# Kernel optimization log

Hardware: AMD Instinct MI355X
Metric: run time of the kernel (lower is better)

The kernel has to match this reference:

```python
import jax, jax.numpy as jnp
import numpy as np
from jax import lax

DIM = 128
TOPW = 4
SCALE = DIM ** (-0.5)


def setup_inputs() -> dict:
    key = jax.random.key(0)
    kq, ki = jax.random.split(key)
    query = jax.random.normal(kq, (4, 4096, DIM), dtype=jnp.float32)
    image = jax.random.normal(ki, (4, 8192, DIM), dtype=jnp.float32)
    return {"query": query, "image": image}


def reference(query, image):
    # diff_routing=False: inputs are detached in torch; no effect on fwd values.
    # attn: (b, Nq, mn) = scaled QK^T
    attn = jnp.einsum('bqc,bmc->bqm', query, image) * SCALE
    _, topw_index = lax.top_k(attn, TOPW)  # (b, Nq, topw)
    return topw_index
```

## Files before the change

kernel.cpp:

```cpp
#include <hip/hip_runtime.h>
#include <float.h>
#include <stdint.h>


#define NBATCH 4
#define NQ 4096
#define NM 8192
#define KD 128

typedef unsigned short ushort_t;
typedef __attribute__((ext_vector_type(8))) short bf16x8;
typedef __attribute__((ext_vector_type(4))) float f32x4;

#define BETTER64(v, i, w, j) (((v) > (w)) || ((v) == (w) && (i) < (j)))

__device__ inline float fmed3(float a, float b, float c) {
#if __has_builtin(__builtin_amdgcn_fmed3f)
  return __builtin_amdgcn_fmed3f(a, b, c);
#else
  return fmaxf(fminf(a, b), fminf(fmaxf(a, b), c));
#endif
}

__device__ inline ushort_t f2bf(float f) {
  unsigned u = __float_as_uint(f);
  u += 0x7fffu + ((u >> 16) & 1u);
  return (ushort_t)(u >> 16);
}

__device__ inline unsigned pk2(float a, float b) {
  return (unsigned)f2bf(a) | ((unsigned)f2bf(b) << 16);
}

__global__ __launch_bounds__(256) void wr_cvt(const float* __restrict__ qry,
                                              const float* __restrict__ img,
                                              ushort_t* __restrict__ qb,
                                              int4* __restrict__ ib) {
  const int t = (int)blockIdx.x * 256 + (int)threadIdx.x;
  if (t < 524288) {
    const int b = t >> 17;
    const int tt = t & 131071;
    const int tile = tt >> 9;
    const int n = tt & 511;
    const int l = n & 63;
    const int m = tile * 32 + (n >> 8) * 16 + (l & 15);
    const int k0 = ((n >> 6) & 3) * 32 + ((l >> 4) & 3) * 8;
    const float* src = img + ((size_t)(b * NM + m)) * KD + k0;
    const float4 v0 = *(const float4*)(src);
    const float4 v1 = *(const float4*)(src + 4);
    int4 o;
    o.x = (int)pk2(v0.x, v0.y);
    o.y = (int)pk2(v0.z, v0.w);
    o.z = (int)pk2(v1.x, v1.y);
    o.w = (int)pk2(v1.z, v1.w);
    ib[t] = o;
  } else {
    const int u = t - 524288;
    const float4 v0 = ((const float4*)qry)[2 * u];
    const float4 v1 = ((const float4*)qry)[2 * u + 1];
    int4 o;
    o.x = (int)pk2(v0.x, v0.y);
    o.y = (int)pk2(v0.z, v0.w);
    o.z = (int)pk2(v1.x, v1.y);
    o.w = (int)pk2(v1.z, v1.w);
    ((int4*)qb)[u] = o;
  }
}

__global__ __launch_bounds__(512, 1) void wr_mfma(const float* __restrict__ qry,
                                                  const float* __restrict__ img,
                                                  const ushort_t* __restrict__ qb,
                                                  const int4* __restrict__ ib,
                                                  int* __restrict__ out) {
  const int bid = (int)blockIdx.x;
  const int b = (bid & 7) >> 1;
  const int qt = ((bid >> 3) << 1) | (bid & 1);
  const int qbase = qt * 64;

  const int tid = (int)threadIdx.x;
  const int lane = tid & 63;
  const int w = tid >> 6;
  const int q15 = lane & 15;
  const int quad = lane >> 4;

  const ushort_t* Qb = qb + ((size_t)b * NQ + qbase) * KD;
  const int4* ibc = ib + (size_t)b * 131072;

  bf16x8 bfrag[4][4];
#pragma unroll
  for (int s = 0; s < 4; ++s)
#pragma unroll
    for (int ks = 0; ks < 4; ++ks)
      bfrag[s][ks] =
          *(const bf16x8*)(Qb + (size_t)(s * 16 + q15) * KD + ks * 32 + quad * 8);

  float tch[4][4];
#pragma unroll
  for (int s = 0; s < 4; ++s)
#pragma unroll
    for (int e = 0; e < 4; ++e) tch[s][e] = -FLT_MAX;

  bf16x8 B0[4], B1[4], B2[4];

  auto loadH = [&](bf16x8* R, int h) {
    const int4* p = ibc + (((w * 64 + h) << 8) + lane);
#pragma unroll
    for (int ks = 0; ks < 4; ++ks) R[ks] = *(const bf16x8*)(p + ks * 64);
  };

  int hl = 3;
  int vb = 2047 - 4 * quad;

  auto step = [&](bf16x8* R) {
    f32x4 a[4];
#pragma unroll
    for (int s = 0; s < 4; ++s) a[s] = {0.f, 0.f, 0.f, 0.f};
#pragma unroll
    for (int ks = 0; ks < 4; ++ks)
#pragma unroll
      for (int s = 0; s < 4; ++s)
        a[s] = __builtin_amdgcn_mfma_f32_16x16x32_bf16(R[ks], bfrag[s][ks], a[s],
                                                       0, 0, 0);
    if (hl < 64) loadH(R, hl);
    ++hl;
#pragma unroll
    for (int s = 0; s < 4; ++s) {
#pragma unroll
      for (int r = 0; r < 4; ++r) {
        const unsigned kr = (unsigned)(vb - r);
        const float k =
            __uint_as_float((__float_as_uint(a[s][r]) & 0xFFFFF800u) | kr);
        tch[s][3] = fmed3(k, tch[s][2], tch[s][3]);
        tch[s][2] = fmed3(k, tch[s][1], tch[s][2]);
        tch[s][1] = fmed3(k, tch[s][0], tch[s][1]);
        tch[s][0] = fmaxf(tch[s][0], k);
      }
    }
    vb -= 16;
  };

  loadH(B0, 0);
  loadH(B1, 1);
  loadH(B2, 2);
  for (int g = 0; g < 21; ++g) { step(B0); step(B1); step(B2); }
  step(B0);

#pragma unroll
  for (int s = 0; s < 4; ++s) {
    float k4[4];
#pragma unroll
    for (int e = 0; e < 4; ++e) k4[e] = __shfl_down(tch[s][e], 32, 64);
#pragma unroll
    for (int e = 0; e < 4; ++e) {
      const float k = k4[e];
      tch[s][3] = fmed3(k, tch[s][2], tch[s][3]);
      tch[s][2] = fmed3(k, tch[s][1], tch[s][2]);
      tch[s][1] = fmed3(k, tch[s][0], tch[s][1]);
      tch[s][0] = fmaxf(tch[s][0], k);
    }
#pragma unroll
    for (int e = 0; e < 4; ++e) k4[e] = __shfl_down(tch[s][e], 16, 64);
#pragma unroll
    for (int e = 0; e < 4; ++e) {
      const float k = k4[e];
      tch[s][3] = fmed3(k, tch[s][2], tch[s][3]);
      tch[s][2] = fmed3(k, tch[s][1], tch[s][2]);
      tch[s][1] = fmed3(k, tch[s][0], tch[s][1]);
      tch[s][0] = fmaxf(tch[s][0], k);
    }
  }

  __shared__ float ck[64][33];
  __shared__ int top8[64][8];
  __shared__ double pd[64][8];
  __shared__ int pi[64][8];

  if (lane < 16) {
#pragma unroll
    for (int s = 0; s < 4; ++s)
#pragma unroll
      for (int e = 0; e < 4; ++e) ck[s * 16 + q15][w * 4 + e] = tch[s][e];
  }
  __syncthreads();

  for (int p = tid; p < 2048; p += 512) {
    const int q = p >> 5;
    const int j = p & 31;
    const float k = ck[q][j];
    int rank = 0;
#pragma unroll 8
    for (int i = 0; i < 32; ++i) {
      const float o = ck[q][i];
      rank += (o > k) || (o == k && i < j);
    }
    if (rank < 8) {
      const unsigned bits = __float_as_uint(k);
      top8[q][rank] = (j >> 2) * 1024 + 2047 - (int)(bits & 0x7FFu);
    }
  }
  __syncthreads();

  {
    const int q = tid >> 3;
    const int slot = tid & 7;
    const int m = top8[q][slot];
    const float* qrow = qry + ((size_t)b * NQ + qbase + q) * KD;
    const float* irow = img + ((size_t)b * NM + m) * KD;
    double s0 = 0.0, s1 = 0.0, s2 = 0.0, s3 = 0.0;
#pragma unroll
    for (int k = 0; k < KD; k += 4) {
      const float4 xv = *(const float4*)(qrow + k);
      const float4 yv = *(const float4*)(irow + k);
      s0 = fma((double)xv.x, (double)yv.x, s0);
      s1 = fma((double)xv.y, (double)yv.y, s1);
      s2 = fma((double)xv.z, (double)yv.z, s2);
      s3 = fma((double)xv.w, (double)yv.w, s3);
    }
    pd[q][slot] = (s0 + s1) + (s2 + s3);
    pi[q][slot] = m;
  }
  __syncthreads();

  if (tid < 64) {
    const int q = tid;
    double fv[4];
    int fi[4];
#pragma unroll
    for (int e = 0; e < 4; ++e) { fv[e] = -DBL_MAX; fi[e] = 0x7fffffff; }
    for (int sl = 0; sl < 8; ++sl) {
      const double v = pd[q][sl];
      const int m = pi[q][sl];
      const bool b0 = BETTER64(v, m, fv[0], fi[0]);
      const bool b1 = BETTER64(v, m, fv[1], fi[1]);
      const bool b2 = BETTER64(v, m, fv[2], fi[2]);
      const bool b3 = BETTER64(v, m, fv[3], fi[3]);
      fv[3] = b2 ? fv[2] : (b3 ? v : fv[3]);
      fi[3] = b2 ? fi[2] : (b3 ? m : fi[3]);
      fv[2] = b1 ? fv[1] : (b2 ? v : fv[2]);
      fi[2] = b1 ? fi[1] : (b2 ? m : fi[2]);
      fv[1] = b0 ? fv[0] : (b1 ? v : fv[1]);
      fi[1] = b0 ? fi[0] : (b1 ? m : fi[1]);
      fv[0] = b0 ? v : fv[0];
      fi[0] = b0 ? m : fi[0];
    }
    int4 o;
    o.x = fi[0]; o.y = fi[1]; o.z = fi[2]; o.w = fi[3];
    *(int4*)(out + ((size_t)b * NQ + qbase + q) * 4) = o;
  }
}

#define QT 64
#define MT 128
#define KC 64
#define NTHREADS 512

__global__ __launch_bounds__(NTHREADS) void wr_main(const float* __restrict__ qry,
                                                    const float* __restrict__ img,
                                                    int* __restrict__ out) {
  __shared__ __align__(16) float A_lds[KD * QT];
  __shared__ __align__(16) float B_lds[KC * MT];

  const int t = (int)threadIdx.x;
  const int b = (int)blockIdx.x >> 6;
  const int qbase = ((int)blockIdx.x & 63) * QT;

  const float* qp = qry + ((size_t)b * NQ + qbase) * KD;
  const float* ip = img + (size_t)b * NM * KD;

  {
    const int r = t >> 3;
    const int kc = t & 7;
    const float* src = qp + (size_t)r * KD;
#pragma unroll
    for (int i = 0; i < 4; ++i) {
      const int k0 = kc * 4 + i * 32;
      const float4 v = *(const float4*)(src + k0);
      A_lds[(k0 + 0) * QT + r] = v.x;
      A_lds[(k0 + 1) * QT + r] = v.y;
      A_lds[(k0 + 2) * QT + r] = v.z;
      A_lds[(k0 + 3) * QT + r] = v.w;
    }
  }

  const int qi = t >> 5;
  const int mi = t & 31;

  float tv[4][4];
  int ti[4][4];
#pragma unroll
  for (int j = 0; j < 4; ++j)
#pragma unroll
    for (int s = 0; s < 4; ++s) { tv[j][s] = -FLT_MAX; ti[j][s] = 0x7fffffff; }

  for (int tile = 0; tile < NM / MT; ++tile) {
    const int mbase = tile * MT;
    float acc[4][4];
#pragma unroll
    for (int j = 0; j < 4; ++j)
#pragma unroll
      for (int s = 0; s < 4; ++s) acc[j][s] = 0.0f;

    for (int kb = 0; kb < KD; kb += KC) {
      __syncthreads();
      {
        const int r = t >> 2;
        const int kc = t & 3;
        const float* src = ip + (size_t)(mbase + r) * KD + kb;
#pragma unroll
        for (int i = 0; i < 4; ++i) {
          const int k0 = kc * 4 + i * 16;
          const float4 v = *(const float4*)(src + k0);
          B_lds[(k0 + 0) * MT + r] = v.x;
          B_lds[(k0 + 1) * MT + r] = v.y;
          B_lds[(k0 + 2) * MT + r] = v.z;
          B_lds[(k0 + 3) * MT + r] = v.w;
        }
      }
      __syncthreads();

#pragma unroll 8
      for (int k = 0; k < KC; ++k) {
        const float4 av = *(const float4*)&A_lds[(kb + k) * QT + qi * 4];
        const float4 bv = *(const float4*)&B_lds[k * MT + mi * 4];
        acc[0][0] = fmaf(av.x, bv.x, acc[0][0]);
        acc[0][1] = fmaf(av.x, bv.y, acc[0][1]);
        acc[0][2] = fmaf(av.x, bv.z, acc[0][2]);
        acc[0][3] = fmaf(av.x, bv.w, acc[0][3]);
        acc[1][0] = fmaf(av.y, bv.x, acc[1][0]);
        acc[1][1] = fmaf(av.y, bv.y, acc[1][1]);
        acc[1][2] = fmaf(av.y, bv.z, acc[1][2]);
        acc[1][3] = fmaf(av.y, bv.w, acc[1][3]);
        acc[2][0] = fmaf(av.z, bv.x, acc[2][0]);
        acc[2][1] = fmaf(av.z, bv.y, acc[2][1]);
        acc[2][2] = fmaf(av.z, bv.z, acc[2][2]);
        acc[2][3] = fmaf(av.z, bv.w, acc[2][3]);
        acc[3][0] = fmaf(av.w, bv.x, acc[3][0]);
        acc[3][1] = fmaf(av.w, bv.y, acc[3][1]);
        acc[3][2] = fmaf(av.w, bv.z, acc[3][2]);
        acc[3][3] = fmaf(av.w, bv.w, acc[3][3]);
      }
    }

#pragma unroll
    for (int j = 0; j < 4; ++j) {
#pragma unroll
      for (int s = 0; s < 4; ++s) {
        const float v = acc[j][s];
        const int m = mbase + mi * 4 + s;
        const bool b0 = v > tv[j][0];
        const bool b1 = v > tv[j][1];
        const bool b2 = v > tv[j][2];
        const bool b3 = v > tv[j][3];
        tv[j][3] = b2 ? tv[j][2] : (b3 ? v : tv[j][3]);
        ti[j][3] = b2 ? ti[j][2] : (b3 ? m : ti[j][3]);
        tv[j][2] = b1 ? tv[j][1] : (b2 ? v : tv[j][2]);
        ti[j][2] = b1 ? ti[j][1] : (b2 ? m : ti[j][2]);
        tv[j][1] = b0 ? tv[j][0] : (b1 ? v : tv[j][1]);
        ti[j][1] = b0 ? ti[j][0] : (b1 ? m : ti[j][1]);
        tv[j][0] = b0 ? v : tv[j][0];
        ti[j][0] = b0 ? m : ti[j][0];
      }
    }
  }

  __syncthreads();
  int* idx_lds = (int*)B_lds;
#pragma unroll
  for (int j = 0; j < 4; ++j)
#pragma unroll
    for (int s = 0; s < 4; ++s)
      idx_lds[(qi * 4 + j) * 128 + mi * 4 + s] = ti[j][s];
  __syncthreads();

  double* pv = (double*)A_lds;
  int* piL = (int*)(A_lds + 4096);
  {
    const int r = t >> 3;
    const int slot = t & 7;
    const float* qrow = qp + (size_t)r * KD;
    double bv[4];
    int bi[4];
#pragma unroll
    for (int e = 0; e < 4; ++e) { bv[e] = -DBL_MAX; bi[e] = 0x7fffffff; }

    for (int c = 0; c < 16; ++c) {
      const int m = idx_lds[r * 128 + slot * 16 + c];
      const float* irow = ip + (size_t)m * KD;
      double s0 = 0.0, s1 = 0.0, s2 = 0.0, s3 = 0.0;
#pragma unroll
      for (int k = 0; k < KD; k += 4) {
        const float4 xv = *(const float4*)(qrow + k);
        const float4 yv = *(const float4*)(irow + k);
        s0 = fma((double)xv.x, (double)yv.x, s0);
        s1 = fma((double)xv.y, (double)yv.y, s1);
        s2 = fma((double)xv.z, (double)yv.z, s2);
        s3 = fma((double)xv.w, (double)yv.w, s3);
      }
      const double v = (s0 + s1) + (s2 + s3);
      const bool b0 = BETTER64(v, m, bv[0], bi[0]);
      const bool b1 = BETTER64(v, m, bv[1], bi[1]);
      const bool b2 = BETTER64(v, m, bv[2], bi[2]);
      const bool b3 = BETTER64(v, m, bv[3], bi[3]);
      bv[3] = b2 ? bv[2] : (b3 ? v : bv[3]);
      bi[3] = b2 ? bi[2] : (b3 ? m : bi[3]);
      bv[2] = b1 ? bv[1] : (b2 ? v : bv[2]);
      bi[2] = b1 ? bi[1] : (b2 ? m : bi[2]);
      bv[1] = b0 ? bv[0] : (b1 ? v : bv[1]);
      bi[1] = b0 ? bi[0] : (b1 ? m : bi[1]);
      bv[0] = b0 ? v : bv[0];
      bi[0] = b0 ? m : bi[0];
    }
#pragma unroll
    for (int e = 0; e < 4; ++e) {
      pv[t * 4 + e] = bv[e];
      piL[t * 4 + e] = bi[e];
    }
  }
  __syncthreads();

  if (t < QT) {
    double fv[4];
    int fi[4];
#pragma unroll
    for (int e = 0; e < 4; ++e) { fv[e] = -DBL_MAX; fi[e] = 0x7fffffff; }
    for (int sl = 0; sl < 8; ++sl) {
#pragma unroll
      for (int e = 0; e < 4; ++e) {
        const double v = pv[(t * 8 + sl) * 4 + e];
        const int m = piL[(t * 8 + sl) * 4 + e];
        const bool b0 = BETTER64(v, m, fv[0], fi[0]);
        const bool b1 = BETTER64(v, m, fv[1], fi[1]);
        const bool b2 = BETTER64(v, m, fv[2], fi[2]);
        const bool b3 = BETTER64(v, m, fv[3], fi[3]);
        fv[3] = b2 ? fv[2] : (b3 ? v : fv[3]);
        fi[3] = b2 ? fi[2] : (b3 ? m : fi[3]);
        fv[2] = b1 ? fv[1] : (b2 ? v : fv[2]);
        fi[2] = b1 ? fi[1] : (b2 ? m : fi[2]);
        fv[1] = b0 ? fv[0] : (b1 ? v : fv[1]);
        fi[1] = b0 ? fi[0] : (b1 ? m : fi[1]);
        fv[0] = b0 ? v : fv[0];
        fi[0] = b0 ? m : fi[0];
      }
    }
    int4 o;
    o.x = fi[0]; o.y = fi[1]; o.z = fi[2]; o.w = fi[3];
    *(int4*)(out + ((size_t)b * NQ + qbase + t) * 4) = o;
  }
}

extern "C" void kernel_launch(void* const* d_in, const int* in_sizes, int n_in,
                              void* d_out, int out_size, void* d_ws, size_t ws_size,
                              hipStream_t stream) {
  const float* qry = (const float*)d_in[0];
  const float* img = (const float*)d_in[1];
  int* out = (int*)d_out;

  const size_t qbBytes = (size_t)NBATCH * NQ * KD * sizeof(ushort_t);
  const size_t ibBytes = (size_t)NBATCH * NM * KD * sizeof(ushort_t);

  if (ws_size >= qbBytes + ibBytes) {
    ushort_t* qb = (ushort_t*)d_ws;
    int4* ib = (int4*)((char*)d_ws + qbBytes);
    wr_cvt<<<3072, 256, 0, stream>>>(qry, img, qb, ib);
    wr_mfma<<<256, 512, 0, stream>>>(qry, img, qb, ib, out);
  } else {
    wr_main<<<NBATCH * (NQ / QT), NTHREADS, 0, stream>>>(qry, img, out);
  }
}
```

Baseline: 133.6 us.

## Fuse bf16 conversion and MFMA top-k kernels with a grid-wide barrier

Merges the separate fp32-to-bf16 conversion kernel into the MFMA top-k kernel. All 256 blocks first convert a slice of the query and image data, then meet at a software grid barrier built from atomics in workspace memory before starting the matmul phase. This removes one kernel launch and the gap between launches. In exchange it adds a hipMemsetAsync per call and relies on all 256 blocks being resident at the same time, otherwise the barrier would deadlock.

Result: slower. 241.4 us (+80.7%).

```diff
diff --git a/kernel.cpp b/kernel.cpp
--- a/kernel.cpp
+++ b/kernel.cpp
@@ -32,12 +32,17 @@
   return (unsigned)f2bf(a) | ((unsigned)f2bf(b) << 16);
 }
 
-__global__ __launch_bounds__(256) void wr_cvt(const float* __restrict__ qry,
-                                              const float* __restrict__ img,
-                                              ushort_t* __restrict__ qb,
-                                              int4* __restrict__ ib) {
-  const int t = (int)blockIdx.x * 256 + (int)threadIdx.x;
-  if (t < 524288) {
+__global__ __launch_bounds__(512, 1) void wr_fused(
+    const float* __restrict__ qry, const float* __restrict__ img,
+    ushort_t* __restrict__ qb, int4* __restrict__ ib,
+    int* __restrict__ bar,
+    int* __restrict__ out) {
+  const int bid = (int)blockIdx.x;
+  const int tid = (int)threadIdx.x;
+
+#pragma unroll
+  for (int i = 0; i < 4; ++i) {
+    const int t = i * 131072 + bid * 512 + tid;
     const int b = t >> 17;
     const int tt = t & 131071;
     const int tile = tt >> 9;
@@ -54,8 +59,10 @@
     o.z = (int)pk2(v1.x, v1.y);
     o.w = (int)pk2(v1.z, v1.w);
     ib[t] = o;
-  } else {
-    const int u = t - 524288;
+  }
+#pragma unroll
+  for (int i = 0; i < 2; ++i) {
+    const int u = i * 131072 + bid * 512 + tid;
     const float4 v0 = ((const float4*)qry)[2 * u];
     const float4 v1 = ((const float4*)qry)[2 * u + 1];
     int4 o;
@@ -65,19 +72,31 @@
     o.w = (int)pk2(v1.z, v1.w);
     ((int4*)qb)[u] = o;
   }
-}
-
-__global__ __launch_bounds__(512, 1) void wr_mfma(const float* __restrict__ qry,
-                                                  const float* __restrict__ img,
-                                                  const ushort_t* __restrict__ qb,
-                                                  const int4* __restrict__ ib,
-                                                  int* __restrict__ out) {
-  const int bid = (int)blockIdx.x;
+
+  __threadfence();
+  __syncthreads();
+  if (tid == 0) {
+    int* cnt = bar;
+    int* flag = bar + 1;
+    const int g = __hip_atomic_load(flag, __ATOMIC_ACQUIRE, __HIP_MEMORY_SCOPE_AGENT);
+    const int old =
+        __hip_atomic_fetch_add(cnt, 1, __ATOMIC_ACQ_REL, __HIP_MEMORY_SCOPE_AGENT);
+    if (old == (int)gridDim.x - 1) {
+      __hip_atomic_store(cnt, 0, __ATOMIC_RELAXED, __HIP_MEMORY_SCOPE_AGENT);
+      __hip_atomic_store(flag, g + 1, __ATOMIC_RELEASE, __HIP_MEMORY_SCOPE_AGENT);
+    } else {
+      while (__hip_atomic_load(flag, __ATOMIC_ACQUIRE, __HIP_MEMORY_SCOPE_AGENT) == g) {
+        __builtin_amdgcn_s_sleep(1);
+      }
+    }
+  }
+  __syncthreads();
+  __threadfence();
+
   const int b = (bid & 7) >> 1;
   const int qt = ((bid >> 3) << 1) | (bid & 1);
   const int qbase = qt * 64;
 
-  const int tid = (int)threadIdx.x;
   const int lane = tid & 63;
   const int w = tid >> 6;
   const int q15 = lane & 15;
@@ -458,11 +477,12 @@
   const size_t qbBytes = (size_t)NBATCH * NQ * KD * sizeof(ushort_t);
   const size_t ibBytes = (size_t)NBATCH * NM * KD * sizeof(ushort_t);
 
-  if (ws_size >= qbBytes + ibBytes) {
+  if (ws_size >= qbBytes + ibBytes + 64) {
     ushort_t* qb = (ushort_t*)d_ws;
     int4* ib = (int4*)((char*)d_ws + qbBytes);
-    wr_cvt<<<3072, 256, 0, stream>>>(qry, img, qb, ib);
-    wr_mfma<<<256, 512, 0, stream>>>(qry, img, qb, ib, out);
+    int* bar = (int*)((char*)d_ws + qbBytes + ibBytes);
+    hipMemsetAsync(bar, 0, 2 * sizeof(int), stream);
+    wr_fused<<<256, 512, 0, stream>>>(qry, img, qb, ib, bar, out);
   } else {
     wr_main<<<NBATCH * (NQ / QT), NTHREADS, 0, stream>>>(qry, img, out);
   }
```

## Switch score GEMM to 32x32x16 MFMA with matching pre-swizzled operand layouts

Applied to the files above, without the earlier changes.

Replaces the 16x16x32 bf16 MFMA tiling with 32x32x16 MFMA, computing two 32-query tiles per 32-image-row step. The conversion kernel now writes both image and query bf16 buffers in the fragment order the new MFMA expects, so operand loads become fully coalesced int4 reads. The aim is fewer MFMA issues and a cheaper cross-lane reduction, with one xor shuffle instead of two shuffles. The cost is larger accumulator register use and a double buffer in place of the previous triple buffer for image prefetch.

After: 130.8 us (median of 3 runs). 2.1% less time.

```diff
diff --git a/kernel.cpp b/kernel.cpp
--- a/kernel.cpp
+++ b/kernel.cpp
@@ -11,6 +11,7 @@
 typedef unsigned short ushort_t;
 typedef __attribute__((ext_vector_type(8))) short bf16x8;
 typedef __attribute__((ext_vector_type(4))) float f32x4;
+typedef __attribute__((ext_vector_type(16))) float f32x16;
 
 #define BETTER64(v, i, w, j) (((v) > (w)) || ((v) == (w) && (i) < (j)))
 
@@ -34,17 +35,19 @@
 
 __global__ __launch_bounds__(256) void wr_cvt(const float* __restrict__ qry,
                                               const float* __restrict__ img,
-                                              ushort_t* __restrict__ qb,
+                                              int4* __restrict__ qb,
                                               int4* __restrict__ ib) {
   const int t = (int)blockIdx.x * 256 + (int)threadIdx.x;
   if (t < 524288) {
     const int b = t >> 17;
     const int tt = t & 131071;
-    const int tile = tt >> 9;
-    const int n = tt & 511;
-    const int l = n & 63;
-    const int m = tile * 32 + (n >> 8) * 16 + (l & 15);
-    const int k0 = ((n >> 6) & 3) * 32 + ((l >> 4) & 3) * 8;
+    const int e = tt >> 14;
+    const int r = tt & 16383;
+    const int tile = r >> 9;
+    const int ks = (r >> 6) & 7;
+    const int l = r & 63;
+    const int m = e * 1024 + tile * 32 + (l & 31);
+    const int k0 = ks * 16 + (l >> 5) * 8;
     const float* src = img + ((size_t)(b * NM + m)) * KD + k0;
     const float4 v0 = *(const float4*)(src);
     const float4 v1 = *(const float4*)(src + 4);
@@ -56,20 +59,30 @@
     ib[t] = o;
   } else {
     const int u = t - 524288;
-    const float4 v0 = ((const float4*)qry)[2 * u];
-    const float4 v1 = ((const float4*)qry)[2 * u + 1];
+    const int b = u >> 16;
+    const int uu = u & 65535;
+    const int qt = uu >> 10;
+    const int r = uu & 1023;
+    const int h = r >> 9;
+    const int ks = (r >> 6) & 7;
+    const int l = r & 63;
+    const int q = qt * 64 + h * 32 + (l & 31);
+    const int k0 = ks * 16 + (l >> 5) * 8;
+    const float* src = qry + ((size_t)(b * NQ + q)) * KD + k0;
+    const float4 v0 = *(const float4*)(src);
+    const float4 v1 = *(const float4*)(src + 4);
     int4 o;
     o.x = (int)pk2(v0.x, v0.y);
     o.y = (int)pk2(v0.z, v0.w);
     o.z = (int)pk2(v1.x, v1.y);
     o.w = (int)pk2(v1.z, v1.w);
-    ((int4*)qb)[u] = o;
+    qb[u] = o;
   }
 }
 
 __global__ __launch_bounds__(512, 1) void wr_mfma(const float* __restrict__ qry,
                                                   const float* __restrict__ img,
-                                                  const ushort_t* __restrict__ qb,
+                                                  const int4* __restrict__ qb,
                                                   const int4* __restrict__ ib,
                                                   int* __restrict__ out) {
   const int bid = (int)blockIdx.x;
@@ -80,93 +93,86 @@
   const int tid = (int)threadIdx.x;
   const int lane = tid & 63;
   const int w = tid >> 6;
-  const int q15 = lane & 15;
-  const int quad = lane >> 4;
-
-  const ushort_t* Qb = qb + ((size_t)b * NQ + qbase) * KD;
-  const int4* ibc = ib + (size_t)b * 131072;
-
-  bf16x8 bfrag[4][4];
-#pragma unroll
-  for (int s = 0; s < 4; ++s)
-#pragma unroll
-    for (int ks = 0; ks < 4; ++ks)
-      bfrag[s][ks] =
-          *(const bf16x8*)(Qb + (size_t)(s * 16 + q15) * KD + ks * 32 + quad * 8);
-
-  float tch[4][4];
-#pragma unroll
-  for (int s = 0; s < 4; ++s)
-#pragma unroll
-    for (int e = 0; e < 4; ++e) tch[s][e] = -FLT_MAX;
-
-  bf16x8 B0[4], B1[4], B2[4];
-
-  auto loadH = [&](bf16x8* R, int h) {
-    const int4* p = ibc + (((w * 64 + h) << 8) + lane);
-#pragma unroll
-    for (int ks = 0; ks < 4; ++ks) R[ks] = *(const bf16x8*)(p + ks * 64);
+  const int l31 = lane & 31;
+  const int lh = lane >> 5;
+
+  const int4* Qb = qb + (size_t)b * 65536 + qt * 1024;
+  const int4* ibc = ib + (size_t)b * 131072 + w * 16384;
+
+  bf16x8 bfrag[2][8];
+#pragma unroll
+  for (int h = 0; h < 2; ++h)
+#pragma unroll
+    for (int ks = 0; ks < 8; ++ks)
+      bfrag[h][ks] = *(const bf16x8*)&Qb[h * 512 + ks * 64 + lane];
+
+  float tch[2][4];
+#pragma unroll
+  for (int c = 0; c < 2; ++c)
+#pragma unroll
+    for (int e = 0; e < 4; ++e) tch[c][e] = -FLT_MAX;
+
+  bf16x8 A0[8], A1[8];
+
+  auto loadA = [&](bf16x8* A, int t) {
+    const int4* p = ibc + t * 512 + lane;
+#pragma unroll
+    for (int ks = 0; ks < 8; ++ks) A[ks] = *(const bf16x8*)&p[ks * 64];
   };
 
-  int hl = 3;
-  int vb = 2047 - 4 * quad;
-
-  auto step = [&](bf16x8* R) {
-    f32x4 a[4];
-#pragma unroll
-    for (int s = 0; s < 4; ++s) a[s] = {0.f, 0.f, 0.f, 0.f};
-#pragma unroll
-    for (int ks = 0; ks < 4; ++ks)
-#pragma unroll
-      for (int s = 0; s < 4; ++s)
-        a[s] = __builtin_amdgcn_mfma_f32_16x16x32_bf16(R[ks], bfrag[s][ks], a[s],
-                                                       0, 0, 0);
-    if (hl < 64) loadH(R, hl);
+  const f32x16 z16 = {0.f, 0.f, 0.f, 0.f, 0.f, 0.f, 0.f, 0.f,
+                      0.f, 0.f, 0.f, 0.f, 0.f, 0.f, 0.f, 0.f};
+
+  int hl = 2;
+  int vbase = 2047 - 4 * lh;
+
+  auto step = [&](bf16x8* A) {
+    f32x16 c0 = __builtin_amdgcn_mfma_f32_32x32x16_bf16(A[0], bfrag[0][0], z16,
+                                                        0, 0, 0);
+    f32x16 c1 = __builtin_amdgcn_mfma_f32_32x32x16_bf16(A[0], bfrag[1][0], z16,
+                                                        0, 0, 0);
+#pragma unroll
+    for (int ks = 1; ks < 8; ++ks) {
+      c0 = __builtin_amdgcn_mfma_f32_32x32x16_bf16(A[ks], bfrag[0][ks], c0,
+                                                   0, 0, 0);
+      c1 = __builtin_amdgcn_mfma_f32_32x32x16_bf16(A[ks], bfrag[1][ks], c1,
+                                                   0, 0, 0);
+    }
+    if (hl < 32) loadA(A, hl);
     ++hl;
 #pragma unroll
-    for (int s = 0; s < 4; ++s) {
-#pragma unroll
-      for (int r = 0; r < 4; ++r) {
-        const unsigned kr = (unsigned)(vb - r);
-        const float k =
-            __uint_as_float((__float_as_uint(a[s][r]) & 0xFFFFF800u) | kr);
-        tch[s][3] = fmed3(k, tch[s][2], tch[s][3]);
-        tch[s][2] = fmed3(k, tch[s][1], tch[s][2]);
-        tch[s][1] = fmed3(k, tch[s][0], tch[s][1]);
-        tch[s][0] = fmaxf(tch[s][0], k);
-      }
-    }
-    vb -= 16;
+    for (int rg = 0; rg < 16; ++rg) {
+      const unsigned kr = (unsigned)(vbase - ((rg & 3) + 8 * (rg >> 2)));
+      float k = __uint_as_float((__float_as_uint(c0[rg]) & 0xFFFFF800u) | kr);
+      tch[0][3] = fmed3(k, tch[0][2], tch[0][3]);
+      tch[0][2] = fmed3(k, tch[0][1], tch[0][2]);
+      tch[0][1] = fmed3(k, tch[0][0], tch[0][1]);
+      tch[0][0] = fmaxf(tch[0][0], k);
+      k = __uint_as_float((__float_as_uint(c1[rg]) & 0xFFFFF800u) | kr);
+      tch[1][3] = fmed3(k, tch[1][2], tch[1][3]);
+      tch[1][2] = fmed3(k, tch[1][1], tch[1][2]);
+      tch[1][1] = fmed3(k, tch[1][0], tch[1][1]);
+      tch[1][0] = fmaxf(tch[1][0], k);
+    }
+    vbase -= 32;
   };
 
-  loadH(B0, 0);
-  loadH(B1, 1);
-  loadH(B2, 2);
-  for (int g = 0; g < 21; ++g) { step(B0); step(B1); step(B2); }
-  step(B0);
-
-#pragma unroll
-  for (int s = 0; s < 4; ++s) {
+  loadA(A0, 0);
+  loadA(A1, 1);
+  for (int g = 0; g < 16; ++g) { step(A0); step(A1); }
+
+#pragma unroll
+  for (int c = 0; c < 2; ++c) {
     float k4[4];
 #pragma unroll
-    for (int e = 0; e < 4; ++e) k4[e] = __shfl_down(tch[s][e], 32, 64);
+    for (int e = 0; e < 4; ++e) k4[e] = __shfl_xor(tch[c][e], 32, 64);
 #pragma unroll
     for (int e = 0; e < 4; ++e) {
       const float k = k4[e];
-      tch[s][3] = fmed3(k, tch[s][2], tch[s][3]);
-      tch[s][2] = fmed3(k, tch[s][1], tch[s][2]);
-      tch[s][1] = fmed3(k, tch[s][0], tch[s][1]);
-      tch[s][0] = fmaxf(tch[s][0], k);
-    }
-#pragma unroll
-    for (int e = 0; e < 4; ++e) k4[e] = __shfl_down(tch[s][e], 16, 64);
-#pragma unroll
-    for (int e = 0; e < 4; ++e) {
-      const float k = k4[e];
-      tch[s][3] = fmed3(k, tch[s][2], tch[s][3]);
-      tch[s][2] = fmed3(k, tch[s][1], tch[s][2]);
-      tch[s][1] = fmed3(k, tch[s][0], tch[s][1]);
-      tch[s][0] = fmaxf(tch[s][0], k);
+      tch[c][3] = fmed3(k, tch[c][2], tch[c][3]);
+      tch[c][2] = fmed3(k, tch[c][1], tch[c][2]);
+      tch[c][1] = fmed3(k, tch[c][0], tch[c][1]);
+      tch[c][0] = fmaxf(tch[c][0], k);
     }
   }
 
@@ -175,11 +181,11 @@
   __shared__ double pd[64][8];
   __shared__ int pi[64][8];
 
-  if (lane < 16) {
-#pragma unroll
-    for (int s = 0; s < 4; ++s)
-#pragma unroll
-      for (int e = 0; e < 4; ++e) ck[s * 16 + q15][w * 4 + e] = tch[s][e];
+  if (lane < 32) {
+#pragma unroll
+    for (int c = 0; c < 2; ++c)
+#pragma unroll
+      for (int e = 0; e < 4; ++e) ck[c * 32 + l31][w * 4 + e] = tch[c][e];
   }
   __syncthreads();
 
@@ -459,7 +465,7 @@
   const size_t ibBytes = (size_t)NBATCH * NM * KD * sizeof(ushort_t);
 
   if (ws_size >= qbBytes + ibBytes) {
-    ushort_t* qb = (ushort_t*)d_ws;
+    int4* qb = (int4*)d_ws;
     int4* ib = (int4*)((char*)d_ws + qbBytes);
     wr_cvt<<<3072, 256, 0, stream>>>(qry, img, qb, ib);
     wr_mfma<<<256, 512, 0, stream>>>(qry, img, qb, ib, out);
```
